# Kernel optimization log

Hardware: AMD Instinct MI355X
Metric: run time of the kernel (lower is better)

The kernel has to match this reference:

```python
import jax, jax.numpy as jnp
import numpy as np

B = 1024        # number of graphs in batch
NNODES = 64     # nodes per graph
NODE = 4        # node feature size
EDGEF = 2       # edge feature size
HID = 32        # hidden_dim
NFACT = 3       # num_factories
NE = 1024       # edges per graph (self.edges list length)


def setup_inputs() -> dict:
    key = jax.random.key(0)
    ks = jax.random.split(key, 12)
    rng = np.random.default_rng(1)
    # per-graph edge list (self.edges in the torch module)
    edges = rng.integers(0, NNODES, size=(NE, 2))
    edges_src = jnp.asarray(edges[:, 0], dtype=jnp.int32)   # [NE]
    edges_dst = jnp.asarray(edges[:, 1], dtype=jnp.int32)   # [NE]
    # batched edge_index for EdgeConv: same per-graph edges offset by b*NNODES
    offs = np.arange(B, dtype=np.int64)[:, None] * NNODES   # [B,1]
    ei_src = (edges[:, 0][None, :] + offs).reshape(-1)
    ei_dst = (edges[:, 1][None, :] + offs).reshape(-1)
    edge_index = jnp.asarray(np.stack([ei_src, ei_dst], 0), dtype=jnp.int32)  # [2, B*NE]

    N = B * NNODES
    E = B * NE
    x = jax.random.normal(ks[0], (N, NODE), dtype=jnp.float32)
    edge_attr = jax.random.normal(ks[1], (E, EDGEF), dtype=jnp.float32)
    action = jax.random.uniform(ks[2], (B, NE + NFACT), dtype=jnp.float32)

    s = 0.1
    W1 = jax.random.normal(ks[3], (2 * NODE + EDGEF, HID), dtype=jnp.float32) * s
    b1 = jnp.zeros((HID,), jnp.float32)
    W2 = jax.random.normal(ks[4], (HID, HID), dtype=jnp.float32) * s
    b2 = jnp.zeros((HID,), jnp.float32)
    D = (NODE + HID) * 2 + 1  # 73
    Wl = jax.random.normal(ks[5], (D, HID), dtype=jnp.float32) * s
    bl = jnp.zeros((HID,), jnp.float32)
    Wv = jax.random.normal(ks[6], (HID, 1), dtype=jnp.float32) * s
    bv = jnp.zeros((1,), jnp.float32)

    return {"x": x, "edge_index": edge_index, "edge_attr": edge_attr,
            "action": action, "edges_src": edges_src, "edges_dst": edges_dst,
            "W1": W1, "b1": b1, "W2": W2, "b2": b2,
            "Wl": Wl, "bl": bl, "Wv": Wv, "bv": bv}


def reference(x, edge_index, edge_attr, action, edges_src, edges_dst,
              W1, b1, W2, b2, Wl, bl, Wv, bv):
    N = x.shape[0]
    src = edge_index[0]  # flow='target_to_source': x_i = x[src], aggregate at src
    dst = edge_index[1]
    # EdgeConv message: MLP(cat[x_i, x_j, edge_attr])
    tmp = jnp.concatenate([x[src], x[dst], edge_attr], axis=1)  # [E, 10]
    msg = jax.nn.relu(tmp @ W1 + b1) @ W2 + b2                  # [E, HID]
    x_pp = jax.ops.segment_sum(msg, src, num_segments=N)        # scatter-add
    # concat node feats with conv output, split into graphs
    h = jnp.concatenate([x, x_pp], axis=1).reshape(B, NNODES, NODE + HID)  # [B,NN,36]
    # gather per-edge endpoint features
    ef = jnp.concatenate([h[:, edges_src], h[:, edges_dst]], axis=2)       # [B,NE,72]
    # factory features: last NFACT nodes duplicated
    pf = jnp.concatenate([h[:, -NFACT:], h[:, -NFACT:]], axis=-1)          # [B,NF,72]
    feats = jnp.concatenate([ef, pf], axis=1)                               # [B,NE+NF,72]
    concat = jnp.concatenate([feats, action[..., None]], axis=-1)           # [B,NE+NF,73]
    hidden = jax.nn.relu(concat @ Wl + bl)                                  # [B,NE+NF,HID]
    v = hidden @ Wv + bv                                                    # [B,NE+NF,1]
    return jnp.sum(v, axis=1).squeeze(-1)                                   # [B]
```

## Files before the change

### kernel.cpp

```cpp
#include <hip/hip_runtime.h>

#define NNODES 64
#define HID 32
#define NFACT 3
#define NE 1024
#define NROWS (NE + NFACT)
#define TPB 256
#define STR 36
#define MAXTILES 128
#define EPT (NE / TPB)

typedef short bf16x8 __attribute__((ext_vector_type(8)));
typedef float f32x2  __attribute__((ext_vector_type(2)));
typedef float f32x4v __attribute__((ext_vector_type(4)));
typedef float f32x16 __attribute__((ext_vector_type(16)));

__device__ __forceinline__ unsigned pack_bf2(float lo, float hi) {
    unsigned ul = __builtin_bit_cast(unsigned, lo);
    unsigned uh = __builtin_bit_cast(unsigned, hi);
    ul += 0x7fffu + ((ul >> 16) & 1u);
    uh += 0x7fffu + ((uh >> 16) & 1u);
    return (ul >> 16) | (uh & 0xffff0000u);
}
__device__ __forceinline__ short f2bf(float f) {
    unsigned u = __builtin_bit_cast(unsigned, f);
    u += 0x7fffu + ((u >> 16) & 1u);
    return (short)(u >> 16);
}
__device__ __forceinline__ float4 fma4(float a, float4 w, float4 c) {
    c.x = fmaf(a, w.x, c.x); c.y = fmaf(a, w.y, c.y);
    c.z = fmaf(a, w.z, c.z); c.w = fmaf(a, w.w, c.w);
    return c;
}
__device__ __forceinline__ f32x2 lo2(float4 v) { return f32x2{v.x, v.y}; }
__device__ __forceinline__ f32x2 hi2(float4 v) { return f32x2{v.z, v.w}; }
__device__ __forceinline__ f32x2 relu2(f32x2 v) {
    return __builtin_elementwise_max(v, f32x2{0.f, 0.f});
}

__global__ __launch_bounds__(TPB, 4) void critic_fused(
    const float* __restrict__ x,
    const float* __restrict__ edge_attr,
    const float* __restrict__ action,
    const int*   __restrict__ es,
    const int*   __restrict__ ed,
    const float* __restrict__ W1,
    const float* __restrict__ b1,
    const float* __restrict__ W2,
    const float* __restrict__ b2,
    const float* __restrict__ Wl,
    const float* __restrict__ bl,
    const float* __restrict__ Wv,
    const float* __restrict__ bv,
    float* __restrict__ out)
{
    const int b    = blockIdx.x;
    const int tid  = threadIdx.x;
    const int lane = tid & 63;
    const int wv   = tid >> 6;
    const int quad = lane >> 4;
    const int m16  = lane & 15;
    const int kh   = quad * 8;

    __shared__ __align__(16) float4 xs4[NNODES];
    __shared__ __align__(16) float  xpp[NNODES * STR];
    __shared__ __align__(16) float  qp0[NNODES * STR];
    __shared__ __align__(16) float  qp1[NNODES * STR];
    __shared__ __align__(16) float  W1s[10 * HID];
    __shared__ float  b1s[HID];
    __shared__ float  wred[TPB / 64];
    __shared__ int    sdeg[NNODES], soff[NNODES], scnt[NNODES];
    __shared__ int    tns[MAXTILES];
    __shared__ int    pep[MAXTILES * 16];
    __shared__ int    snt;

    if (tid < NNODES) { xs4[tid] = ((const float4*)x)[b * NNODES + tid]; sdeg[tid] = 0; scnt[tid] = 0; }
    if (tid < 80) ((float4*)W1s)[tid] = ((const float4*)W1)[tid];
    if (tid < HID) b1s[tid] = b1[tid];
    if (tid < MAXTILES) tns[tid] = 0;
#pragma unroll
    for (int i = 0; i < MAXTILES * 16 / TPB; i++) pep[tid + i * TPB] = 0xFFF;
#pragma unroll 1
    for (int i = tid; i < NNODES * STR; i += TPB) xpp[i] = 0.0f;

    int ces[EPT], ced[EPT];
#pragma unroll
    for (int i = 0; i < EPT; i++) {
        ces[i] = es[tid + i * TPB];
        ced[i] = ed[tid + i * TPB];
    }
    __syncthreads();

#pragma unroll
    for (int i = 0; i < EPT; i++) atomicAdd(&sdeg[ces[i]], 1);
    {
        const int n  = lane;
        const int k0 = wv * 8;
        const float4 xv = xs4[n];
        const float4* b1v = (const float4*)&b1s[k0];
        float4 q1a = b1v[0], q1b = b1v[1];
        float4 q2a = make_float4(0.f, 0.f, 0.f, 0.f), q2b = q2a;
#pragma unroll 1
        for (int i = 0; i < 4; i++) {
            const float xi = (i == 0) ? xv.x : (i == 1) ? xv.y : (i == 2) ? xv.z : xv.w;
            const float4* wa = (const float4*)&W1s[i * HID + k0];
            const float4* wb = (const float4*)&W1s[(4 + i) * HID + k0];
            q1a = fma4(xi, wa[0], q1a); q1b = fma4(xi, wa[1], q1b);
            q2a = fma4(xi, wb[0], q2a); q2b = fma4(xi, wb[1], q2b);
        }
        float4* q1w = (float4*)&qp0[n * STR + k0];
        float4* q2w = (float4*)&qp1[n * STR + k0];
        q1w[0] = q1a; q1w[1] = q1b;
        q2w[0] = q2a; q2w[1] = q2b;
    }
    __syncthreads();

    if (tid < NNODES) {
        const int cnt = (sdeg[tid] + 15) >> 4;
        int scan = cnt;
#pragma unroll
        for (int o = 1; o < 64; o <<= 1) {
            const int v = __shfl_up(scan, o);
            if (tid >= o) scan += v;
        }
        const int base = scan - cnt;
        soff[tid] = base;
        if (tid == NNODES - 1) snt = scan;
#pragma unroll 1
        for (int j = 0; j < cnt; j++) tns[base + j] = tid;
    }
    __syncthreads();

#pragma unroll
    for (int i = 0; i < EPT; i++) {
        const int n = ces[i];
        const int idx = atomicAdd(&scnt[n], 1);
        pep[soff[n] * 16 + idx] = (tid + i * TPB) | (ced[i] << 12) | (n << 18);
    }
    __syncthreads();

    {
        const float2* ea2 = (const float2*)edge_attr + (size_t)b * NE;
        const int NW  = TPB / 64;
        const int klo = (lane >> 5) * 8;
        const int n32 = lane & 31;

        const float4* w8l = (const float4*)&W1s[8 * HID + klo];
        const float4* w8h = (const float4*)&W1s[8 * HID + 16 + klo];
        const float4* w9l = (const float4*)&W1s[9 * HID + klo];
        const float4* w9h = (const float4*)&W1s[9 * HID + 16 + klo];
        const f32x2 w8_0 = lo2(w8l[0]), w8_1 = hi2(w8l[0]), w8_2 = lo2(w8l[1]), w8_3 = hi2(w8l[1]);
        const f32x2 w8_4 = lo2(w8h[0]), w8_5 = hi2(w8h[0]), w8_6 = lo2(w8h[1]), w8_7 = hi2(w8h[1]);
        const f32x2 w9_0 = lo2(w9l[0]), w9_1 = hi2(w9l[0]), w9_2 = lo2(w9l[1]), w9_3 = hi2(w9l[1]);
        const f32x2 w9_4 = lo2(w9h[0]), w9_5 = hi2(w9h[0]), w9_6 = lo2(w9h[1]), w9_7 = hi2(w9h[1]);

        bf16x8 bfA, bfB;
#pragma unroll
        for (int j = 0; j < 8; j++) {
            bfA[j] = f2bf(W2[(klo + j) * HID + n32]);
            bfB[j] = f2bf(W2[(16 + klo + j) * HID + n32]);
        }

        const int np = (snt + 1) >> 1;

        int raws[16];
#pragma unroll
        for (int i = 0; i < 16; i++)
            raws[i] = pep[(wv + i * NW) * 32 + n32];

#pragma unroll
        for (int i = 0; i < 16; i++) {
            const int p = wv + i * NW;
            if (p < np) {
                const int raw = raws[i];
                const int tA  = tns[2 * p];
                const int tB  = tns[2 * p + 1];
                const int e    = raw & 0xFFF;
                const bool pad = (e == 0xFFF);
                const int d0   = (raw >> 12) & 63;
                const int nd   = (raw >> 18) & 63;
                const float2 ea = ea2[pad ? 0 : e];
                const f32x2 eax = {ea.x, ea.x};
                const f32x2 eay = {ea.y, ea.y};

                const float4* A1 = (const float4*)&qp0[nd * STR + klo];
                const float4* A2 = (const float4*)&qp0[nd * STR + 16 + klo];
                const float4* G1 = (const float4*)&qp1[d0 * STR + klo];
                const float4* G2 = (const float4*)&qp1[d0 * STR + 16 + klo];
                const float4 a0 = A1[0], a1 = A1[1], a2 = A2[0], a3 = A2[1];
                const float4 g0 = G1[0], g1 = G1[1], g2 = G2[0], g3 = G2[1];

                const f32x2 hA0 = relu2(lo2(a0) + lo2(g0) + eax * w8_0 + eay * w9_0);
                const f32x2 hA1 = relu2(hi2(a0) + hi2(g0) + eax * w8_1 + eay * w9_1);
                const f32x2 hA2 = relu2(lo2(a1) + lo2(g1) + eax * w8_2 + eay * w9_2);
                const f32x2 hA3 = relu2(hi2(a1) + hi2(g1) + eax * w8_3 + eay * w9_3);
                const f32x2 hB0 = relu2(lo2(a2) + lo2(g2) + eax * w8_4 + eay * w9_4);
                const f32x2 hB1 = relu2(hi2(a2) + hi2(g2) + eax * w8_5 + eay * w9_5);
                const f32x2 hB2 = relu2(lo2(a3) + lo2(g3) + eax * w8_6 + eay * w9_6);
                const f32x2 hB3 = relu2(hi2(a3) + hi2(g3) + eax * w8_7 + eay * w9_7);

                uint4 pkA, pkB;
                pkA.x = pad ? 0u : pack_bf2(hA0.x, hA0.y);
                pkA.y = pad ? 0u : pack_bf2(hA1.x, hA1.y);
                pkA.z = pad ? 0u : pack_bf2(hA2.x, hA2.y);
                pkA.w = pad ? 0u : pack_bf2(hA3.x, hA3.y);
                pkB.x = pad ? 0u : pack_bf2(hB0.x, hB0.y);
                pkB.y = pad ? 0u : pack_bf2(hB1.x, hB1.y);
                pkB.z = pad ? 0u : pack_bf2(hB2.x, hB2.y);
                pkB.w = pad ? 0u : pack_bf2(hB3.x, hB3.y);
                const bf16x8 afA = __builtin_bit_cast(bf16x8, pkA);
                const bf16x8 afB = __builtin_bit_cast(bf16x8, pkB);

                f32x16 c;
#pragma unroll
                for (int j = 0; j < 16; j++) c[j] = 0.0f;
                c = __builtin_amdgcn_mfma_f32_32x32x16_bf16(afA, bfA, c, 0, 0, 0);
                c = __builtin_amdgcn_mfma_f32_32x32x16_bf16(afB, bfB, c, 0, 0, 0);

                float sA = ((c[0] + c[1]) + (c[2] + c[3])) + ((c[4] + c[5]) + (c[6] + c[7]));
                float sB = ((c[8] + c[9]) + (c[10] + c[11])) + ((c[12] + c[13]) + (c[14] + c[15]));
                sA += __shfl_xor(sA, 32);
                sB += __shfl_xor(sB, 32);
                const int   nst = (lane < 32) ? tA : tB;
                const float sv  = (lane < 32) ? sA : sB;
                atomicAdd(&xpp[nst * STR + n32], sv);
            }
        }
    }
    __syncthreads();

    bf16x8 bP1a, bP1b, bP2a, bP2b;
#pragma unroll
    for (int j = 0; j < 8; j++) {
        bP1a[j] = f2bf(Wl[(4 + kh + j) * HID + m16]);
        bP1b[j] = f2bf(Wl[(4 + kh + j) * HID + 16 + m16]);
        bP2a[j] = f2bf(Wl[(40 + kh + j) * HID + m16]);
        bP2b[j] = f2bf(Wl[(40 + kh + j) * HID + 16 + m16]);
    }
    float wx1a[4], wx1b[4], wx2a[4], wx2b[4];
#pragma unroll
    for (int i = 0; i < 4; i++) {
        wx1a[i] = Wl[i * HID + m16];
        wx1b[i] = Wl[i * HID + 16 + m16];
        wx2a[i] = Wl[(36 + i) * HID + m16];
        wx2b[i] = Wl[(36 + i) * HID + 16 + m16];
    }
    const float blca = bl[m16], blcb = bl[16 + m16];
    float b2k[8];
#pragma unroll
    for (int j = 0; j < 8; j++) b2k[j] = b2[kh + j];
    const int   mrow = wv * 16 + m16;
    const float dn   = (float)sdeg[mrow];

    {
        const float4* xr = (const float4*)&xpp[mrow * STR + kh];
        float4 x0 = xr[0], x1 = xr[1];
        x0.x = fmaf(dn, b2k[0], x0.x); x0.y = fmaf(dn, b2k[1], x0.y);
        x0.z = fmaf(dn, b2k[2], x0.z); x0.w = fmaf(dn, b2k[3], x0.w);
        x1.x = fmaf(dn, b2k[4], x1.x); x1.y = fmaf(dn, b2k[5], x1.y);
        x1.z = fmaf(dn, b2k[6], x1.z); x1.w = fmaf(dn, b2k[7], x1.w);
        uint4 packed;
        packed.x = pack_bf2(x0.x, x0.y);
        packed.y = pack_bf2(x0.z, x0.w);
        packed.z = pack_bf2(x1.x, x1.y);
        packed.w = pack_bf2(x1.z, x1.w);
        const bf16x8 af = __builtin_bit_cast(bf16x8, packed);

        f32x4v c1a, c1b, c2a, c2b;
#pragma unroll
        for (int r = 0; r < 4; r++) {
            const float4 xv = xs4[wv * 16 + quad * 4 + r];
            float a0 = blca, a1 = blcb, a2 = 0.f, a3 = 0.f;
#pragma unroll
            for (int i = 0; i < 4; i++) {
                const float xi = (i == 0) ? xv.x : (i == 1) ? xv.y : (i == 2) ? xv.z : xv.w;
                a0 = fmaf(xi, wx1a[i], a0);
                a1 = fmaf(xi, wx1b[i], a1);
                a2 = fmaf(xi, wx2a[i], a2);
                a3 = fmaf(xi, wx2b[i], a3);
            }
            c1a[r] = a0; c1b[r] = a1; c2a[r] = a2; c2b[r] = a3;
        }
        c1a = __builtin_amdgcn_mfma_f32_16x16x32_bf16(af, bP1a, c1a, 0, 0, 0);
        c1b = __builtin_amdgcn_mfma_f32_16x16x32_bf16(af, bP1b, c1b, 0, 0, 0);
        c2a = __builtin_amdgcn_mfma_f32_16x16x32_bf16(af, bP2a, c2a, 0, 0, 0);
        c2b = __builtin_amdgcn_mfma_f32_16x16x32_bf16(af, bP2b, c2b, 0, 0, 0);

#pragma unroll
        for (int r = 0; r < 4; r++) {
            const int row = wv * 16 + quad * 4 + r;
            qp0[row * STR + m16]      = c1a[r];
            qp0[row * STR + 16 + m16] = c1b[r];
            qp1[row * STR + m16]      = c2a[r];
            qp1[row * STR + 16 + m16] = c2b[r];
        }
    }
    __syncthreads();

    float vsum = 0.0f;
    {
        const float* actb = action + (size_t)b * NROWS;
        const float bvv = bv[0];
        const f32x2* w72v = (const f32x2*)(Wl + 72 * HID);
        const f32x2* wvv  = (const f32x2*)Wv;
#pragma unroll 1
        for (int i = 0; i < 4; i += 2) {
            const int naA = ces[i],     nbA = ced[i];
            const int naB = ces[i + 1], nbB = ced[i + 1];
            const float aA = actb[tid + i * TPB];
            const float aB = actb[tid + (i + 1) * TPB];
            const f32x2 avA = {aA, aA}, avB = {aB, aB};
            const float4* p1A = (const float4*)&qp0[naA * STR];
            const float4* p2A = (const float4*)&qp1[nbA * STR];
            const float4* p1B = (const float4*)&qp0[naB * STR];
            const float4* p2B = (const float4*)&qp1[nbB * STR];
            f32x2 vaccA = {0.f, 0.f}, vaccB = {0.f, 0.f};
#pragma unroll 2
            for (int q = 0; q < 8; q++) {
                const float4 paA = p1A[q], pbA = p2A[q];
                const float4 paB = p1B[q], pbB = p2B[q];
                const f32x2 rLA = relu2(lo2(paA) + lo2(pbA) + avA * w72v[2 * q]);
                const f32x2 rHA = relu2(hi2(paA) + hi2(pbA) + avA * w72v[2 * q + 1]);
                const f32x2 rLB = relu2(lo2(paB) + lo2(pbB) + avB * w72v[2 * q]);
                const f32x2 rHB = relu2(hi2(paB) + hi2(pbB) + avB * w72v[2 * q + 1]);
                vaccA += rLA * wvv[2 * q] + rHA * wvv[2 * q + 1];
                vaccB += rLB * wvv[2 * q] + rHB * wvv[2 * q + 1];
            }
            vsum += (bvv + vaccA.x + vaccA.y) + (bvv + vaccB.x + vaccB.y);
        }
        if (tid < NFACT) {
            const int r = NE + tid;
            const int na = NNODES - NFACT + tid;
            const float a = actb[r];
            const f32x2 av = {a, a};
            const float4* p1v = (const float4*)&qp0[na * STR];
            const float4* p2v = (const float4*)&qp1[na * STR];
            f32x2 vacc = {0.f, 0.f};
#pragma unroll 1
            for (int q = 0; q < 8; q++) {
                const float4 pa = p1v[q], pb = p2v[q];
                const f32x2 rL = relu2(lo2(pa) + lo2(pb) + av * w72v[2 * q]);
                const f32x2 rH = relu2(hi2(pa) + hi2(pb) + av * w72v[2 * q + 1]);
                vacc += rL * wvv[2 * q] + rH * wvv[2 * q + 1];
            }
            vsum += bvv + vacc.x + vacc.y;
        }
    }

#pragma unroll
    for (int off = 32; off > 0; off >>= 1)
        vsum += __shfl_down(vsum, off, 64);
    if ((tid & 63) == 0) wred[tid >> 6] = vsum;
    __syncthreads();
    if (tid == 0) {
        float t = 0.0f;
#pragma unroll
        for (int w = 0; w < TPB / 64; w++) t += wred[w];
        out[b] = t;
    }
}

extern "C" void kernel_launch(void* const* d_in, const int* in_sizes, int n_in,
                              void* d_out, int out_size, void* d_ws, size_t ws_size,
                              hipStream_t stream) {
    const float* x         = (const float*)d_in[0];
    const float* edge_attr = (const float*)d_in[2];
    const float* action    = (const float*)d_in[3];
    const int*   es        = (const int*)d_in[4];
    const int*   ed        = (const int*)d_in[5];
    const float* W1        = (const float*)d_in[6];
    const float* b1        = (const float*)d_in[7];
    const float* W2        = (const float*)d_in[8];
    const float* b2        = (const float*)d_in[9];
    const float* Wl        = (const float*)d_in[10];
    const float* bl        = (const float*)d_in[11];
    const float* Wv        = (const float*)d_in[12];
    const float* bv        = (const float*)d_in[13];
    float* out = (float*)d_out;

    critic_fused<<<dim3(out_size), dim3(TPB), 0, stream>>>(
        x, edge_attr, action, es, ed, W1, b1, W2, b2, Wl, bl, Wv, bv, out);
}
```

Measured before the change: 126.8 us.

## Double block size to 512 threads and redistribute per-graph work across waves

Raises threads per block from 256 to 512 and rebalances every phase to match. Each thread now handles 2 edges instead of 4, each wave computes 4 instead of 8 hidden columns in the node projection, each wave processes 8 instead of 16 MFMA edge tiles, and only the first 4 waves run the per-node MFMA stage. The aim is more parallelism per graph and shorter per-thread serial chains. The cost is more idle waves in some phases and heavier register and occupancy limits under the new launch bounds.

```diff
diff --git a/kernel.cpp b/kernel.cpp
--- a/kernel.cpp
+++ b/kernel.cpp
@@ -5,7 +5,8 @@
 #define NFACT 3
 #define NE 1024
 #define NROWS (NE + NFACT)
-#define TPB 256
+#define TPB 512
+#define NW (TPB / 64)
 #define STR 36
 #define MAXTILES 128
 #define EPT (NE / TPB)
@@ -38,7 +39,7 @@
     return __builtin_elementwise_max(v, f32x2{0.f, 0.f});
 }
 
-__global__ __launch_bounds__(TPB, 4) void critic_fused(
+__global__ __launch_bounds__(TPB, 8) void critic_fused(
     const float* __restrict__ x,
     const float* __restrict__ edge_attr,
     const float* __restrict__ action,
@@ -68,7 +69,7 @@
     __shared__ __align__(16) float  qp1[NNODES * STR];
     __shared__ __align__(16) float  W1s[10 * HID];
     __shared__ float  b1s[HID];
-    __shared__ float  wred[TPB / 64];
+    __shared__ float  wred[NW];
     __shared__ int    sdeg[NNODES], soff[NNODES], scnt[NNODES];
     __shared__ int    tns[MAXTILES];
     __shared__ int    pep[MAXTILES * 16];
@@ -95,23 +96,20 @@
     for (int i = 0; i < EPT; i++) atomicAdd(&sdeg[ces[i]], 1);
     {
         const int n  = lane;
-        const int k0 = wv * 8;
+        const int k0 = wv * 4;
         const float4 xv = xs4[n];
-        const float4* b1v = (const float4*)&b1s[k0];
-        float4 q1a = b1v[0], q1b = b1v[1];
-        float4 q2a = make_float4(0.f, 0.f, 0.f, 0.f), q2b = q2a;
+        float4 q1 = ((const float4*)&b1s[k0])[0];
+        float4 q2 = make_float4(0.f, 0.f, 0.f, 0.f);
 #pragma unroll 1
         for (int i = 0; i < 4; i++) {
             const float xi = (i == 0) ? xv.x : (i == 1) ? xv.y : (i == 2) ? xv.z : xv.w;
-            const float4* wa = (const float4*)&W1s[i * HID + k0];
-            const float4* wb = (const float4*)&W1s[(4 + i) * HID + k0];
-            q1a = fma4(xi, wa[0], q1a); q1b = fma4(xi, wa[1], q1b);
-            q2a = fma4(xi, wb[0], q2a); q2b = fma4(xi, wb[1], q2b);
-        }
-        float4* q1w = (float4*)&qp0[n * STR + k0];
-        float4* q2w = (float4*)&qp1[n * STR + k0];
-        q1w[0] = q1a; q1w[1] = q1b;
-        q2w[0] = q2a; q2w[1] = q2b;
+            const float4 wa = ((const float4*)&W1s[i * HID + k0])[0];
+            const float4 wb = ((const float4*)&W1s[(4 + i) * HID + k0])[0];
+            q1 = fma4(xi, wa, q1);
+            q2 = fma4(xi, wb, q2);
+        }
+        ((float4*)&qp0[n * STR + k0])[0] = q1;
+        ((float4*)&qp1[n * STR + k0])[0] = q2;
     }
     __syncthreads();
 
@@ -141,7 +139,6 @@
 
     {
         const float2* ea2 = (const float2*)edge_attr + (size_t)b * NE;
-        const int NW  = TPB / 64;
         const int klo = (lane >> 5) * 8;
         const int n32 = lane & 31;
 
@@ -163,13 +160,13 @@
 
         const int np = (snt + 1) >> 1;
 
-        int raws[16];
-#pragma unroll
-        for (int i = 0; i < 16; i++)
+        int raws[8];
+#pragma unroll
+        for (int i = 0; i < 8; i++)
             raws[i] = pep[(wv + i * NW) * 32 + n32];
 
 #pragma unroll
-        for (int i = 0; i < 16; i++) {
+        for (int i = 0; i < 8; i++) {
             const int p = wv + i * NW;
             if (p < np) {
                 const int raw = raws[i];
@@ -229,30 +226,30 @@
     }
     __syncthreads();
 
-    bf16x8 bP1a, bP1b, bP2a, bP2b;
-#pragma unroll
-    for (int j = 0; j < 8; j++) {
-        bP1a[j] = f2bf(Wl[(4 + kh + j) * HID + m16]);
-        bP1b[j] = f2bf(Wl[(4 + kh + j) * HID + 16 + m16]);
-        bP2a[j] = f2bf(Wl[(40 + kh + j) * HID + m16]);
-        bP2b[j] = f2bf(Wl[(40 + kh + j) * HID + 16 + m16]);
-    }
-    float wx1a[4], wx1b[4], wx2a[4], wx2b[4];
-#pragma unroll
-    for (int i = 0; i < 4; i++) {
-        wx1a[i] = Wl[i * HID + m16];
-        wx1b[i] = Wl[i * HID + 16 + m16];
-        wx2a[i] = Wl[(36 + i) * HID + m16];
-        wx2b[i] = Wl[(36 + i) * HID + 16 + m16];
-    }
-    const float blca = bl[m16], blcb = bl[16 + m16];
-    float b2k[8];
-#pragma unroll
-    for (int j = 0; j < 8; j++) b2k[j] = b2[kh + j];
-    const int   mrow = wv * 16 + m16;
-    const float dn   = (float)sdeg[mrow];
-
-    {
+    if (wv < 4) {
+        bf16x8 bP1a, bP1b, bP2a, bP2b;
+#pragma unroll
+        for (int j = 0; j < 8; j++) {
+            bP1a[j] = f2bf(Wl[(4 + kh + j) * HID + m16]);
+            bP1b[j] = f2bf(Wl[(4 + kh + j) * HID + 16 + m16]);
+            bP2a[j] = f2bf(Wl[(40 + kh + j) * HID + m16]);
+            bP2b[j] = f2bf(Wl[(40 + kh + j) * HID + 16 + m16]);
+        }
+        float wx1a[4], wx1b[4], wx2a[4], wx2b[4];
+#pragma unroll
+        for (int i = 0; i < 4; i++) {
+            wx1a[i] = Wl[i * HID + m16];
+            wx1b[i] = Wl[i * HID + 16 + m16];
+            wx2a[i] = Wl[(36 + i) * HID + m16];
+            wx2b[i] = Wl[(36 + i) * HID + 16 + m16];
+        }
+        const float blca = bl[m16], blcb = bl[16 + m16];
+        float b2k[8];
+#pragma unroll
+        for (int j = 0; j < 8; j++) b2k[j] = b2[kh + j];
+        const int   mrow = wv * 16 + m16;
+        const float dn   = (float)sdeg[mrow];
+
         const float4* xr = (const float4*)&xpp[mrow * STR + kh];
         float4 x0 = xr[0], x1 = xr[1];
         x0.x = fmaf(dn, b2k[0], x0.x); x0.y = fmaf(dn, b2k[1], x0.y);
@@ -303,12 +300,11 @@
         const float bvv = bv[0];
         const f32x2* w72v = (const f32x2*)(Wl + 72 * HID);
         const f32x2* wvv  = (const f32x2*)Wv;
-#pragma unroll 1
-        for (int i = 0; i < 4; i += 2) {
-            const int naA = ces[i],     nbA = ced[i];
-            const int naB = ces[i + 1], nbB = ced[i + 1];
-            const float aA = actb[tid + i * TPB];
-            const float aB = actb[tid + (i + 1) * TPB];
+        {
+            const int naA = ces[0], nbA = ced[0];
+            const int naB = ces[1], nbB = ced[1];
+            const float aA = actb[tid];
+            const float aB = actb[tid + TPB];
             const f32x2 avA = {aA, aA}, avB = {aB, aB};
             const float4* p1A = (const float4*)&qp0[naA * STR];
             const float4* p2A = (const float4*)&qp1[nbA * STR];
@@ -326,7 +322,7 @@
                 vaccA += rLA * wvv[2 * q] + rHA * wvv[2 * q + 1];
                 vaccB += rLB * wvv[2 * q] + rHB * wvv[2 * q + 1];
             }
-            vsum += (bvv + vaccA.x + vaccA.y) + (bvv + vaccB.x + vaccB.y);
+            vsum = (bvv + vaccA.x + vaccA.y) + (bvv + vaccB.x + vaccB.y);
         }
         if (tid < NFACT) {
             const int r = NE + tid;
@@ -355,7 +351,7 @@
     if (tid == 0) {
         float t = 0.0f;
 #pragma unroll
-        for (int w = 0; w < TPB / 64; w++) t += wred[w];
+        for (int w = 0; w < NW; w++) t += wred[w];
         out[b] = t;
     }
 }
```

Measured after the change: 194.3 us. +53.2%, slower.

## Store per-node projection tables as packed bf16 in LDS and raise occupancy

Applied to the files above, without the earlier changes.

The per-node projection tables qp0/qp1 (fp32, stride 36) become packed bf16 tables qh0/qh1 (stride 20 words), used both for the edge-message stage and the final per-edge value stage. This roughly halves LDS footprint and gather bandwidth, and launch bounds are raised to 5 blocks per SM to use the freed LDS. The cost is bf16 rounding of intermediate values, an extra __syncthreads before reusing the buffers, and unpack shifts in the inner loops.

```diff
diff --git a/kernel.cpp b/kernel.cpp
--- a/kernel.cpp
+++ b/kernel.cpp
@@ -7,6 +7,7 @@
 #define NROWS (NE + NFACT)
 #define TPB 256
 #define STR 36
+#define QSTR 20
 #define MAXTILES 128
 #define EPT (NE / TPB)
 
@@ -27,6 +28,10 @@
     u += 0x7fffu + ((u >> 16) & 1u);
     return (short)(u >> 16);
 }
+__device__ __forceinline__ f32x2 ubf2(unsigned u) {
+    return f32x2{__builtin_bit_cast(float, u << 16),
+                 __builtin_bit_cast(float, u & 0xffff0000u)};
+}
 __device__ __forceinline__ float4 fma4(float a, float4 w, float4 c) {
     c.x = fmaf(a, w.x, c.x); c.y = fmaf(a, w.y, c.y);
     c.z = fmaf(a, w.z, c.z); c.w = fmaf(a, w.w, c.w);
@@ -38,7 +43,7 @@
     return __builtin_elementwise_max(v, f32x2{0.f, 0.f});
 }
 
-__global__ __launch_bounds__(TPB, 4) void critic_fused(
+__global__ __launch_bounds__(TPB, 5) void critic_fused(
     const float* __restrict__ x,
     const float* __restrict__ edge_attr,
     const float* __restrict__ action,
@@ -62,11 +67,11 @@
     const int m16  = lane & 15;
     const int kh   = quad * 8;
 
-    __shared__ __align__(16) float4 xs4[NNODES];
-    __shared__ __align__(16) float  xpp[NNODES * STR];
-    __shared__ __align__(16) float  qp0[NNODES * STR];
-    __shared__ __align__(16) float  qp1[NNODES * STR];
-    __shared__ __align__(16) float  W1s[10 * HID];
+    __shared__ __align__(16) float4   xs4[NNODES];
+    __shared__ __align__(16) float    xpp[NNODES * STR];
+    __shared__ __align__(16) unsigned qh0[NNODES * QSTR];
+    __shared__ __align__(16) unsigned qh1[NNODES * QSTR];
+    __shared__ __align__(16) float    W1s[10 * HID];
     __shared__ float  b1s[HID];
     __shared__ float  wred[TPB / 64];
     __shared__ int    sdeg[NNODES], soff[NNODES], scnt[NNODES];
@@ -108,10 +113,13 @@
             q1a = fma4(xi, wa[0], q1a); q1b = fma4(xi, wa[1], q1b);
             q2a = fma4(xi, wb[0], q2a); q2b = fma4(xi, wb[1], q2b);
         }
-        float4* q1w = (float4*)&qp0[n * STR + k0];
-        float4* q2w = (float4*)&qp1[n * STR + k0];
-        q1w[0] = q1a; q1w[1] = q1b;
-        q2w[0] = q2a; q2w[1] = q2b;
+        uint4 p1, p2;
+        p1.x = pack_bf2(q1a.x, q1a.y); p1.y = pack_bf2(q1a.z, q1a.w);
+        p1.z = pack_bf2(q1b.x, q1b.y); p1.w = pack_bf2(q1b.z, q1b.w);
+        p2.x = pack_bf2(q2a.x, q2a.y); p2.y = pack_bf2(q2a.z, q2a.w);
+        p2.z = pack_bf2(q2b.x, q2b.y); p2.w = pack_bf2(q2b.z, q2b.w);
+        *(uint4*)&qh0[n * QSTR + wv * 4] = p1;
+        *(uint4*)&qh1[n * QSTR + wv * 4] = p2;
     }
     __syncthreads();
 
@@ -141,9 +149,10 @@
 
     {
         const float2* ea2 = (const float2*)edge_attr + (size_t)b * NE;
-        const int NW  = TPB / 64;
-        const int klo = (lane >> 5) * 8;
-        const int n32 = lane & 31;
+        const int NW   = TPB / 64;
+        const int klo  = (lane >> 5) * 8;
+        const int klo2 = klo >> 1;
+        const int n32  = lane & 31;
 
         const float4* w8l = (const float4*)&W1s[8 * HID + klo];
         const float4* w8h = (const float4*)&W1s[8 * HID + 16 + klo];
@@ -183,21 +192,19 @@
                 const f32x2 eax = {ea.x, ea.x};
                 const f32x2 eay = {ea.y, ea.y};
 
-                const float4* A1 = (const float4*)&qp0[nd * STR + klo];
-                const float4* A2 = (const float4*)&qp0[nd * STR + 16 + klo];
-                const float4* G1 = (const float4*)&qp1[d0 * STR + klo];
-                const float4* G2 = (const float4*)&qp1[d0 * STR + 16 + klo];
-                const float4 a0 = A1[0], a1 = A1[1], a2 = A2[0], a3 = A2[1];
-                const float4 g0 = G1[0], g1 = G1[1], g2 = G2[0], g3 = G2[1];
-
-                const f32x2 hA0 = relu2(lo2(a0) + lo2(g0) + eax * w8_0 + eay * w9_0);
-                const f32x2 hA1 = relu2(hi2(a0) + hi2(g0) + eax * w8_1 + eay * w9_1);
-                const f32x2 hA2 = relu2(lo2(a1) + lo2(g1) + eax * w8_2 + eay * w9_2);
-                const f32x2 hA3 = relu2(hi2(a1) + hi2(g1) + eax * w8_3 + eay * w9_3);
-                const f32x2 hB0 = relu2(lo2(a2) + lo2(g2) + eax * w8_4 + eay * w9_4);
-                const f32x2 hB1 = relu2(hi2(a2) + hi2(g2) + eax * w8_5 + eay * w9_5);
-                const f32x2 hB2 = relu2(lo2(a3) + lo2(g3) + eax * w8_6 + eay * w9_6);
-                const f32x2 hB3 = relu2(hi2(a3) + hi2(g3) + eax * w8_7 + eay * w9_7);
+                const uint4 A1 = *(const uint4*)&qh0[nd * QSTR + klo2];
+                const uint4 A2 = *(const uint4*)&qh0[nd * QSTR + 8 + klo2];
+                const uint4 G1 = *(const uint4*)&qh1[d0 * QSTR + klo2];
+                const uint4 G2 = *(const uint4*)&qh1[d0 * QSTR + 8 + klo2];
+
+                const f32x2 hA0 = relu2(ubf2(A1.x) + ubf2(G1.x) + eax * w8_0 + eay * w9_0);
+                const f32x2 hA1 = relu2(ubf2(A1.y) + ubf2(G1.y) + eax * w8_1 + eay * w9_1);
+                const f32x2 hA2 = relu2(ubf2(A1.z) + ubf2(G1.z) + eax * w8_2 + eay * w9_2);
+                const f32x2 hA3 = relu2(ubf2(A1.w) + ubf2(G1.w) + eax * w8_3 + eay * w9_3);
+                const f32x2 hB0 = relu2(ubf2(A2.x) + ubf2(G2.x) + eax * w8_4 + eay * w9_4);
+                const f32x2 hB1 = relu2(ubf2(A2.y) + ubf2(G2.y) + eax * w8_5 + eay * w9_5);
+                const f32x2 hB2 = relu2(ubf2(A2.z) + ubf2(G2.z) + eax * w8_6 + eay * w9_6);
+                const f32x2 hB3 = relu2(ubf2(A2.w) + ubf2(G2.w) + eax * w8_7 + eay * w9_7);
 
                 uint4 pkA, pkB;
                 pkA.x = pad ? 0u : pack_bf2(hA0.x, hA0.y);
@@ -286,13 +293,16 @@
         c2a = __builtin_amdgcn_mfma_f32_16x16x32_bf16(af, bP2a, c2a, 0, 0, 0);
         c2b = __builtin_amdgcn_mfma_f32_16x16x32_bf16(af, bP2b, c2b, 0, 0, 0);
 
+        __syncthreads();
+        unsigned short* h0 = (unsigned short*)qh0;
+        unsigned short* h1 = (unsigned short*)qh1;
 #pragma unroll
         for (int r = 0; r < 4; r++) {
-            const int row = wv * 16 + quad * 4 + r;
-            qp0[row * STR + m16]      = c1a[r];
-            qp0[row * STR + 16 + m16] = c1b[r];
-            qp1[row * STR + m16]      = c2a[r];
-            qp1[row * STR + 16 + m16] = c2b[r];
+            const int row = (wv * 16 + quad * 4 + r) * (2 * QSTR);
+            h0[row + m16]      = (unsigned short)f2bf(c1a[r]);
+            h0[row + 16 + m16] = (unsigned short)f2bf(c1b[r]);
+            h1[row + m16]      = (unsigned short)f2bf(c2a[r]);
+            h1[row + 16 + m16] = (unsigned short)f2bf(c2b[r]);
         }
     }
     __syncthreads();
@@ -310,21 +320,24 @@
             const float aA = actb[tid + i * TPB];
             const float aB = actb[tid + (i + 1) * TPB];
             const f32x2 avA = {aA, aA}, avB = {aB, aB};
-            const float4* p1A = (const float4*)&qp0[naA * STR];
-            const float4* p2A = (const float4*)&qp1[nbA * STR];
-            const float4* p1B = (const float4*)&qp0[naB * STR];
-            const float4* p2B = (const float4*)&qp1[nbB * STR];
+            const uint4* p1A = (const uint4*)&qh0[naA * QSTR];
+            const uint4* p2A = (const uint4*)&qh1[nbA * QSTR];
+            const uint4* p1B = (const uint4*)&qh0[naB * QSTR];
+            const uint4* p2B = (const uint4*)&qh1[nbB * QSTR];
             f32x2 vaccA = {0.f, 0.f}, vaccB = {0.f, 0.f};
-#pragma unroll 2
-            for (int q = 0; q < 8; q++) {
-                const float4 paA = p1A[q], pbA = p2A[q];
-                const float4 paB = p1B[q], pbB = p2B[q];
-                const f32x2 rLA = relu2(lo2(paA) + lo2(pbA) + avA * w72v[2 * q]);
-                const f32x2 rHA = relu2(hi2(paA) + hi2(pbA) + avA * w72v[2 * q + 1]);
-                const f32x2 rLB = relu2(lo2(paB) + lo2(pbB) + avB * w72v[2 * q]);
-                const f32x2 rHB = relu2(hi2(paB) + hi2(pbB) + avB * w72v[2 * q + 1]);
-                vaccA += rLA * wvv[2 * q] + rHA * wvv[2 * q + 1];
-                vaccB += rLB * wvv[2 * q] + rHB * wvv[2 * q + 1];
+#pragma unroll
+            for (int g = 0; g < 4; g++) {
+                const uint4 uaA = p1A[g], ubA = p2A[g];
+                const uint4 uaB = p1B[g], ubB = p2B[g];
+                const int j = g * 4;
+                vaccA += relu2(ubf2(uaA.x) + ubf2(ubA.x) + avA * w72v[j + 0]) * wvv[j + 0];
+                vaccA += relu2(ubf2(uaA.y) + ubf2(ubA.y) + avA * w72v[j + 1]) * wvv[j + 1];
+                vaccA += relu2(ubf2(uaA.z) + ubf2(ubA.z) + avA * w72v[j + 2]) * wvv[j + 2];
+                vaccA += relu2(ubf2(uaA.w) + ubf2(ubA.w) + avA * w72v[j + 3]) * wvv[j + 3];
+                vaccB += relu2(ubf2(uaB.x) + ubf2(ubB.x) + avB * w72v[j + 0]) * wvv[j + 0];
+                vaccB += relu2(ubf2(uaB.y) + ubf2(ubB.y) + avB * w72v[j + 1]) * wvv[j + 1];
+                vaccB += relu2(ubf2(uaB.z) + ubf2(ubB.z) + avB * w72v[j + 2]) * wvv[j + 2];
+                vaccB += relu2(ubf2(uaB.w) + ubf2(ubB.w) + avB * w72v[j + 3]) * wvv[j + 3];
             }
             vsum += (bvv + vaccA.x + vaccA.y) + (bvv + vaccB.x + vaccB.y);
         }
@@ -333,15 +346,17 @@
             const int na = NNODES - NFACT + tid;
             const float a = actb[r];
             const f32x2 av = {a, a};
-            const float4* p1v = (const float4*)&qp0[na * STR];
-            const float4* p2v = (const float4*)&qp1[na * STR];
+            const uint4* p1v = (const uint4*)&qh0[na * QSTR];
+            const uint4* p2v = (const uint4*)&qh1[na * QSTR];
             f32x2 vacc = {0.f, 0.f};
-#pragma unroll 1
-            for (int q = 0; q < 8; q++) {
-                const float4 pa = p1v[q], pb = p2v[q];
-                const f32x2 rL = relu2(lo2(pa) + lo2(pb) + av * w72v[2 * q]);
-                const f32x2 rH = relu2(hi2(pa) + hi2(pb) + av * w72v[2 * q + 1]);
-                vacc += rL * wvv[2 * q] + rH * wvv[2 * q + 1];
+#pragma unroll
+            for (int g = 0; g < 4; g++) {
+                const uint4 ua = p1v[g], ub = p2v[g];
+                const int j = g * 4;
+                vacc += relu2(ubf2(ua.x) + ubf2(ub.x) + av * w72v[j + 0]) * wvv[j + 0];
+                vacc += relu2(ubf2(ua.y) + ubf2(ub.y) + av * w72v[j + 1]) * wvv[j + 1];
+                vacc += relu2(ubf2(ua.z) + ubf2(ub.z) + av * w72v[j + 2]) * wvv[j + 2];
+                vacc += relu2(ubf2(ua.w) + ubf2(ub.w) + av * w72v[j + 3]) * wvv[j + 3];
             }
             vsum += bvv + vacc.x + vacc.y;
         }
```

After: 127.8 us. Within noise of the previous version (+0.8%).
